# Performance work log

Measured on AMD Instinct MI355X. Metric: run time of the kernel, lower is better.

Reference implementation:

```python
import jax, jax.numpy as jnp
import numpy as np
import math

NUM_LAYERS = 4
NHEAD = 8
D_MODEL = 256
EPS_ATTN = 1e-6
EPS_LN = 1e-5


def _pos_encoding(d_model, h, w, dtype):
    # LoFTR 2D sinusoidal pos-enc, sliced to (h, w)
    d4 = d_model // 4
    y_pos = jnp.arange(1, h + 1, dtype=dtype)[None, :, None]  # [1,h,1]
    x_pos = jnp.arange(1, w + 1, dtype=dtype)[None, None, :]  # [1,1,w]
    div = jnp.exp(jnp.arange(0, d_model // 2, 2, dtype=dtype) * (-math.log(10000.0) / (d_model // 2)))
    div = div[:, None, None]  # [d4,1,1]
    pe = jnp.zeros((d_model, h, w), dtype=dtype)
    pe = pe.at[0::4].set(jnp.sin(x_pos * div))
    pe = pe.at[1::4].set(jnp.cos(x_pos * div))
    pe = pe.at[2::4].set(jnp.sin(y_pos * div))
    pe = pe.at[3::4].set(jnp.cos(y_pos * div))
    return pe


def _layernorm(x, g, b):
    mu = jnp.mean(x, axis=-1, keepdims=True)
    var = jnp.mean(jnp.square(x - mu), axis=-1, keepdims=True)
    return (x - mu) * jax.lax.rsqrt(var + EPS_LN) * g + b


def _encoder_layer(x, Wq, Wk, Wv, Wm, W1, W2, g1, b1, g2, b2):
    # x: [n, L, d]; weights stored [in, out]
    n, L, d = x.shape
    dh = d // NHEAD
    q = (x @ Wq).reshape(n, L, NHEAD, dh)
    k = (x @ Wk).reshape(n, L, NHEAD, dh)
    v = (x @ Wv).reshape(n, L, NHEAD, dh)
    # linear attention: feature map elu(x)+1
    Q = jax.nn.elu(q) + 1.0
    K = jax.nn.elu(k) + 1.0
    v_len = jnp.asarray(L, x.dtype)
    V = v / v_len
    KV = jnp.einsum('nshd,nshv->nhdv', K, V)            # [n,H,dh,dh]
    Z = 1.0 / (jnp.einsum('nlhd,nhd->nlh', Q, K.sum(axis=1)) + EPS_ATTN)
    msg = jnp.einsum('nlhd,nhdv,nlh->nlhv', Q, KV, Z) * v_len  # [n,L,H,dh]
    msg = msg.reshape(n, L, d) @ Wm
    msg = _layernorm(msg, g1, b1)
    msg = jnp.concatenate([x, msg], axis=-1)             # [n,L,2d]
    msg = jax.nn.relu(msg @ W1) @ W2
    msg = _layernorm(msg, g2, b2)
    return x + msg


def setup_inputs() -> dict:
    key = jax.random.key(0)
    ks = jax.random.split(key, 8)
    b, c, h, w = 8, D_MODEL, 64, 64
    d = D_MODEL
    sc_d = 1.0 / math.sqrt(d)
    sc_2d = 1.0 / math.sqrt(2 * d)
    feats = jax.random.normal(ks[0], (b, c, h, w), dtype=jnp.float32)
    Wq = jax.random.normal(ks[1], (NUM_LAYERS, d, d), dtype=jnp.float32) * sc_d
    Wk = jax.random.normal(ks[2], (NUM_LAYERS, d, d), dtype=jnp.float32) * sc_d
    Wv = jax.random.normal(ks[3], (NUM_LAYERS, d, d), dtype=jnp.float32) * sc_d
    Wmerge = jax.random.normal(ks[4], (NUM_LAYERS, d, d), dtype=jnp.float32) * sc_d
    Wmlp1 = jax.random.normal(ks[5], (NUM_LAYERS, 2 * d, 2 * d), dtype=jnp.float32) * sc_2d
    Wmlp2 = jax.random.normal(ks[6], (NUM_LAYERS, 2 * d, d), dtype=jnp.float32) * sc_2d
    ln1_g = jnp.ones((NUM_LAYERS, d), dtype=jnp.float32)
    ln1_b = jnp.zeros((NUM_LAYERS, d), dtype=jnp.float32)
    ln2_g = jnp.ones((NUM_LAYERS, d), dtype=jnp.float32)
    ln2_b = jnp.zeros((NUM_LAYERS, d), dtype=jnp.float32)
    return {'feats': feats, 'Wq': Wq, 'Wk': Wk, 'Wv': Wv, 'Wmerge': Wmerge,
            'Wmlp1': Wmlp1, 'Wmlp2': Wmlp2, 'ln1_g': ln1_g, 'ln1_b': ln1_b,
            'ln2_g': ln2_g, 'ln2_b': ln2_b}


def reference(feats, Wq, Wk, Wv, Wmerge, Wmlp1, Wmlp2, ln1_g, ln1_b, ln2_g, ln2_b):
    b, c, h, w = feats.shape
    x = feats + _pos_encoding(c, h, w, feats.dtype)[None]   # add_posEnc=True
    x = x.reshape(b, c, h * w).transpose(0, 2, 1)            # n (h w) c
    for i in range(NUM_LAYERS):
        x = _encoder_layer(x, Wq[i], Wk[i], Wv[i], Wmerge[i], Wmlp1[i], Wmlp2[i],
                           ln1_g[i], ln1_b[i], ln2_g[i], ln2_b[i])
    return x.transpose(0, 2, 1).reshape(b, c, h, w)
```

## Files before the change

kernel.cpp:

```cpp
#include <hip/hip_runtime.h>
#include <hip/hip_bf16.h>

#define LTOT 4096
#define DM 256
#define BATCH 8
#define MROWS (BATCH * LTOT)
#define NX ((size_t)MROWS * DM)

typedef __bf16 bf16x8 __attribute__((ext_vector_type(8)));
typedef float f32x4 __attribute__((ext_vector_type(4)));

#define AS1 __attribute__((address_space(1)))
#define AS3 __attribute__((address_space(3)))

__device__ __forceinline__ float elu1(float x) {
    return x > 0.f ? x + 1.f : expf(x);
}
__device__ __forceinline__ ushort f2bf(float f) {
    unsigned u = __float_as_uint(f);
    u += 0x7FFFu + ((u >> 16) & 1u);
    return (ushort)(u >> 16);
}
__device__ __forceinline__ float b2f(ushort u) {
    return __uint_as_float(((unsigned)u) << 16);
}

__global__ __launch_bounds__(256) void prep_kernel(const float* __restrict__ feats,
                                                   ushort* __restrict__ XC) {
    __shared__ float tile[32][33];
    int b = blockIdx.z;
    int l0 = blockIdx.x * 32;
    int c0 = blockIdx.y * 32;
    int tx = threadIdx.x, ty = threadIdx.y;
#pragma unroll
    for (int j = 0; j < 4; ++j) {
        int c = c0 + ty + j * 8;
        tile[ty + j * 8][tx] = feats[((size_t)(b * DM + c)) * LTOT + l0 + tx];
    }
    __syncthreads();
#pragma unroll
    for (int j = 0; j < 4; ++j) {
        int l = l0 + ty + j * 8;
        int c = c0 + tx;
        int i2 = (c >> 2) * 2;
        float dv = expf((float)i2 * -0.07195578415156063f);
        int rem = c & 3;
        int y = l >> 6, xc = l & 63;
        float pos = (rem < 2) ? (float)(xc + 1) : (float)(y + 1);
        float arg = pos * dv;
        float pe = (rem & 1) ? cosf(arg) : sinf(arg);
        float val = tile[tx][ty + j * 8] + pe;
        size_t row = (size_t)(b * LTOT + l);
        XC[row * 512 + c] = f2bf(val);
    }
}

__global__ __launch_bounds__(256) void unprep_kernel(const float* __restrict__ X,
                                                     float* __restrict__ out) {
    __shared__ float tile[32][33];
    int b = blockIdx.z;
    int l0 = blockIdx.x * 32;
    int c0 = blockIdx.y * 32;
    int tx = threadIdx.x, ty = threadIdx.y;
#pragma unroll
    for (int j = 0; j < 4; ++j) {
        int l = l0 + ty + j * 8;
        tile[ty + j * 8][tx] = X[((size_t)(b * LTOT + l)) * DM + c0 + tx];
    }
    __syncthreads();
#pragma unroll
    for (int j = 0; j < 4; ++j) {
        int c = c0 + ty + j * 8;
        out[((size_t)(b * DM + c)) * LTOT + l0 + tx] = tile[tx][ty + j * 8];
    }
}

__global__ __launch_bounds__(256) void wtrans_all(const float* __restrict__ Wq,
                                                  const float* __restrict__ Wk,
                                                  const float* __restrict__ Wv,
                                                  const float* __restrict__ Wm,
                                                  const float* __restrict__ W1,
                                                  const float* __restrict__ W2,
                                                  ushort* __restrict__ WTqkv,
                                                  ushort* __restrict__ WTm,
                                                  ushort* __restrict__ WT1,
                                                  ushort* __restrict__ WT2) {
    __shared__ float t[32][33];
    int idx = blockIdx.x;
    const float* W;
    ushort* WT;
    int K, N, KT, z, r;
    size_t in_ls, out_ls;
    if (idx < 1024) {
        int which = idx >> 8, local = idx & 255;
        K = 256; N = 256; KT = 8; in_ls = 65536;
        if (which == 0)      { W = Wq; WT = WTqkv;          out_ls = 196608; }
        else if (which == 1) { W = Wk; WT = WTqkv + 65536;  out_ls = 196608; }
        else if (which == 2) { W = Wv; WT = WTqkv + 131072; out_ls = 196608; }
        else                 { W = Wm; WT = WTm;            out_ls = 65536; }
        z = local >> 6; r = local & 63;
    } else if (idx < 2048) {
        int local = idx - 1024;
        K = 512; N = 512; KT = 16; in_ls = 262144; out_ls = 262144;
        W = W1; WT = WT1;
        z = local >> 8; r = local & 255;
    } else {
        int local = idx - 2048;
        K = 512; N = 256; KT = 16; in_ls = 131072; out_ls = 131072;
        W = W2; WT = WT2;
        z = local >> 7; r = local & 127;
    }
    int k0 = (r % KT) * 32, n0 = (r / KT) * 32;
    const float* Wz = W + (size_t)z * in_ls;
    ushort* WTz = WT + (size_t)z * out_ls;
    int tx = threadIdx.x & 31, ty = threadIdx.x >> 5;
#pragma unroll
    for (int j = 0; j < 4; ++j)
        t[ty + j * 8][tx] = Wz[(size_t)(k0 + ty + j * 8) * N + n0 + tx];
    __syncthreads();
#pragma unroll
    for (int j = 0; j < 4; ++j)
        WTz[(size_t)(n0 + ty + j * 8) * K + k0 + tx] = f2bf(t[tx][ty + j * 8]);
}

template <int ACT, int K>
__global__ __launch_bounds__(512, 2) void gemm_bf16(const ushort* __restrict__ A, int lda,
                                                    const ushort* __restrict__ Bt,
                                                    ushort* __restrict__ Cb,
                                                    int N) {
    constexpr int S = K / 32;
    __shared__ ushort As[3][4096];
    __shared__ ushort Bs[3][8192];
    int tid = threadIdx.x;
    int m0 = blockIdx.x * 128, n0 = blockIdx.y * 256;
    int wave = tid >> 6, lane = tid & 63;
    int wm = (wave >> 2) * 64, wn = (wave & 3) * 64;
    int fm = lane & 15, kg = lane >> 4;
    int rr = tid >> 2, cc = (tid & 3) * 8;

    const ushort* Ag = A + (size_t)(m0 + rr) * lda + cc;
    const ushort* Bg = Bt + (size_t)(n0 + rr) * K + cc;
    const ushort* Bg2 = Bt + (size_t)(n0 + rr + 128) * K + cc;

    f32x4 acc[4][4] = {};

#define STAGE_G(buf, k0)                                                          \
    do {                                                                          \
        __builtin_amdgcn_global_load_lds((const AS1 void*)(Ag + (k0)),            \
                                         (AS3 void*)(&As[buf][wave * 512]),       \
                                         16, 0, 0);                               \
        __builtin_amdgcn_global_load_lds((const AS1 void*)(Bg + (k0)),            \
                                         (AS3 void*)(&Bs[buf][wave * 512]),       \
                                         16, 0, 0);                               \
        __builtin_amdgcn_global_load_lds((const AS1 void*)(Bg2 + (k0)),           \
                                         (AS3 void*)(&Bs[buf][4096 + wave * 512]),\
                                         16, 0, 0);                               \
    } while (0)

    STAGE_G(0, 0);
    STAGE_G(1, 32);
#pragma unroll
    for (int t = 0; t < S; ++t) {
        if (t + 1 < S) asm volatile("s_waitcnt vmcnt(3)" ::: "memory");
        else           asm volatile("s_waitcnt vmcnt(0)" ::: "memory");
        __builtin_amdgcn_s_barrier();
        const int rb = t % 3;
        bf16x8 afr[4], bfr[4];
#pragma unroll
        for (int i = 0; i < 4; ++i)
            afr[i] = *(const bf16x8*)(&As[rb][(wm + i * 16 + fm) * 32 + kg * 8]);
#pragma unroll
        for (int j = 0; j < 4; ++j)
            bfr[j] = *(const bf16x8*)(&Bs[rb][(wn + j * 16 + fm) * 32 + kg * 8]);
        if (t + 2 < S) STAGE_G((t + 2) % 3, (t + 2) * 32);
#pragma unroll
        for (int i = 0; i < 4; ++i)
#pragma unroll
            for (int j = 0; j < 4; ++j)
                acc[i][j] = __builtin_amdgcn_mfma_f32_16x16x32_bf16(afr[i], bfr[j], acc[i][j], 0, 0, 0);
        asm volatile("" ::: "memory");
        __builtin_amdgcn_s_barrier();
    }
#undef STAGE_G

#pragma unroll
    for (int i = 0; i < 4; ++i) {
        int grow0 = m0 + wm + i * 16 + kg * 4;
#pragma unroll
        for (int r = 0; r < 4; ++r) {
            size_t rowoff = (size_t)(grow0 + r) * N;
#pragma unroll
            for (int j = 0; j < 4; ++j) {
                float v = acc[i][j][r];
                int col = n0 + wn + j * 16 + fm;
                if (ACT == 2) v = fmaxf(v, 0.f);
                if (ACT == 3) v = (col < 512) ? elu1(v) : v;
                Cb[rowoff + col] = f2bf(v);
            }
        }
    }
}

template <int RES, int K>
__global__ __launch_bounds__(512, 2) void gemm_ln(const ushort* __restrict__ A, int lda,
                                                  const ushort* __restrict__ Bt,
                                                  const float* __restrict__ g,
                                                  const float* __restrict__ bta,
                                                  float* __restrict__ Xout,
                                                  ushort* __restrict__ XC) {
    constexpr int S = K / 32;
    __shared__ ushort As[3][4096];
    __shared__ ushort Bs[3][8192];
    __shared__ float red[128 * 8];
    __shared__ float musig[128 * 2];
    int tid = threadIdx.x;
    int m0 = blockIdx.x * 128;
    int wave = tid >> 6, lane = tid & 63;
    int wm = (wave >> 2) * 64, wn = (wave & 3) * 64;
    int fm = lane & 15, kg = lane >> 4;
    int rr = tid >> 2, cc = (tid & 3) * 8;

    const ushort* Ag = A + (size_t)(m0 + rr) * lda + cc;
    const ushort* Bg = Bt + (size_t)rr * K + cc;
    const ushort* Bg2 = Bt + (size_t)(rr + 128) * K + cc;

    f32x4 acc[4][4] = {};

#define STAGE_L(buf, k0)                                                          \
    do {                                                                          \
        __builtin_amdgcn_global_load_lds((const AS1 void*)(Ag + (k0)),            \
                                         (AS3 void*)(&As[buf][wave * 512]),       \
                                         16, 0, 0);                               \
        __builtin_amdgcn_global_load_lds((const AS1 void*)(Bg + (k0)),            \
                                         (AS3 void*)(&Bs[buf][wave * 512]),       \
                                         16, 0, 0);                               \
        __builtin_amdgcn_global_load_lds((const AS1 void*)(Bg2 + (k0)),           \
                                         (AS3 void*)(&Bs[buf][4096 + wave * 512]),\
                                         16, 0, 0);                               \
    } while (0)

    STAGE_L(0, 0);
    STAGE_L(1, 32);
#pragma unroll
    for (int t = 0; t < S; ++t) {
        if (t + 1 < S) asm volatile("s_waitcnt vmcnt(3)" ::: "memory");
        else           asm volatile("s_waitcnt vmcnt(0)" ::: "memory");
        __builtin_amdgcn_s_barrier();
        const int rb = t % 3;
        bf16x8 afr[4], bfr[4];
#pragma unroll
        for (int i = 0; i < 4; ++i)
            afr[i] = *(const bf16x8*)(&As[rb][(wm + i * 16 + fm) * 32 + kg * 8]);
#pragma unroll
        for (int j = 0; j < 4; ++j)
            bfr[j] = *(const bf16x8*)(&Bs[rb][(wn + j * 16 + fm) * 32 + kg * 8]);
        if (t + 2 < S) STAGE_L((t + 2) % 3, (t + 2) * 32);
#pragma unroll
        for (int i = 0; i < 4; ++i)
#pragma unroll
            for (int j = 0; j < 4; ++j)
                acc[i][j] = __builtin_amdgcn_mfma_f32_16x16x32_bf16(afr[i], bfr[j], acc[i][j], 0, 0, 0);
        asm volatile("" ::: "memory");
        __builtin_amdgcn_s_barrier();
    }
#undef STAGE_L

#pragma unroll
    for (int i = 0; i < 4; ++i) {
#pragma unroll
        for (int r = 0; r < 4; ++r) {
            float s = acc[i][0][r] + acc[i][1][r] + acc[i][2][r] + acc[i][3][r];
            float q = acc[i][0][r] * acc[i][0][r] + acc[i][1][r] * acc[i][1][r] +
                      acc[i][2][r] * acc[i][2][r] + acc[i][3][r] * acc[i][3][r];
#pragma unroll
            for (int o = 1; o < 16; o <<= 1) {
                s += __shfl_xor(s, o, 64);
                q += __shfl_xor(q, o, 64);
            }
            if ((lane & 15) == 0) {
                int row = wm + i * 16 + kg * 4 + r;
                red[row * 8 + (wave & 3)] = s;
                red[row * 8 + 4 + (wave & 3)] = q;
            }
        }
    }
    __syncthreads();
    if (tid < 128) {
        float s = red[tid * 8 + 0] + red[tid * 8 + 1] + red[tid * 8 + 2] + red[tid * 8 + 3];
        float q = red[tid * 8 + 4] + red[tid * 8 + 5] + red[tid * 8 + 6] + red[tid * 8 + 7];
        float mu = s * (1.f / 256.f);
        float var = q * (1.f / 256.f) - mu * mu;
        musig[tid * 2] = mu;
        musig[tid * 2 + 1] = rsqrtf(var + 1e-5f);
    }
    __syncthreads();

    float gv[4], bv[4];
#pragma unroll
    for (int j = 0; j < 4; ++j) {
        int col = wn + j * 16 + fm;
        gv[j] = g[col];
        bv[j] = bta[col];
    }
#pragma unroll
    for (int i = 0; i < 4; ++i) {
#pragma unroll
        for (int r = 0; r < 4; ++r) {
            int rl = wm + i * 16 + kg * 4 + r;
            float mu = musig[rl * 2], rstd = musig[rl * 2 + 1];
            size_t grow = (size_t)(m0 + rl);
#pragma unroll
            for (int j = 0; j < 4; ++j) {
                int col = wn + j * 16 + fm;
                float v = (acc[i][j][r] - mu) * rstd * gv[j] + bv[j];
                if (RES) {
                    float x = b2f(XC[grow * 512 + col]) + v;
                    XC[grow * 512 + col] = f2bf(x);
                    if (Xout) Xout[grow * 256 + col] = x;
                } else {
                    XC[grow * 512 + 256 + col] = f2bf(v);
                }
            }
        }
    }
}

__global__ __launch_bounds__(256) void kv_kernel(const ushort* __restrict__ Kf,
                                                 const ushort* __restrict__ Vf,
                                                 int str,
                                                 float* __restrict__ KVp,
                                                 float* __restrict__ KSp) {
    __shared__ float redv[3][8][8][16];
    __shared__ float redk[3][8][4];
    int tid = threadIdx.x;
    int bh = blockIdx.x, sp = blockIdx.y;
    int b = bh >> 3, h = bh & 7;
    int sg = tid >> 6, d2 = (tid >> 3) & 7, v2 = tid & 7;
    size_t rbase = (size_t)(b * LTOT + sp * 512 + sg * 128) * str;
    const ushort* Kp = Kf + rbase + h * 32 + d2 * 4;
    const ushort* Vp = Vf + rbase + h * 32 + v2 * 4;
    float acc[4][4] = {};
    float ks[4] = {};
#pragma unroll 4
    for (int s = 0; s < 128; ++s) {
        ushort4 k4 = *(const ushort4*)(Kp + (size_t)s * str);
        ushort4 v4 = *(const ushort4*)(Vp + (size_t)s * str);
        float kk0 = b2f(k4.x), kk1 = b2f(k4.y), kk2 = b2f(k4.z), kk3 = b2f(k4.w);
        float vv0 = b2f(v4.x), vv1 = b2f(v4.y), vv2 = b2f(v4.z), vv3 = b2f(v4.w);
        acc[0][0] += kk0 * vv0; acc[0][1] += kk0 * vv1; acc[0][2] += kk0 * vv2; acc[0][3] += kk0 * vv3;
        acc[1][0] += kk1 * vv0; acc[1][1] += kk1 * vv1; acc[1][2] += kk1 * vv2; acc[1][3] += kk1 * vv3;
        acc[2][0] += kk2 * vv0; acc[2][1] += kk2 * vv1; acc[2][2] += kk2 * vv2; acc[2][3] += kk2 * vv3;
        acc[3][0] += kk3 * vv0; acc[3][1] += kk3 * vv1; acc[3][2] += kk3 * vv2; acc[3][3] += kk3 * vv3;
        ks[0] += kk0; ks[1] += kk1; ks[2] += kk2; ks[3] += kk3;
    }
    if (sg > 0) {
#pragma unroll
        for (int i = 0; i < 4; ++i)
#pragma unroll
            for (int j = 0; j < 4; ++j)
                redv[sg - 1][d2][v2][i * 4 + j] = acc[i][j];
        if (v2 == 0) {
#pragma unroll
            for (int i = 0; i < 4; ++i) redk[sg - 1][d2][i] = ks[i];
        }
    }
    __syncthreads();
    if (sg == 0) {
#pragma unroll
        for (int t = 0; t < 3; ++t)
#pragma unroll
            for (int i = 0; i < 4; ++i)
#pragma unroll
                for (int j = 0; j < 4; ++j)
                    acc[i][j] += redv[t][d2][v2][i * 4 + j];
        float* base = KVp + (size_t)(sp * 64 + bh) * 1024;
#pragma unroll
        for (int i = 0; i < 4; ++i) {
            float4 o = make_float4(acc[i][0], acc[i][1], acc[i][2], acc[i][3]);
            *(float4*)(base + (d2 * 4 + i) * 32 + v2 * 4) = o;
        }
        if (v2 == 0) {
#pragma unroll
            for (int t = 0; t < 3; ++t)
#pragma unroll
                for (int i = 0; i < 4; ++i) ks[i] += redk[t][d2][i];
#pragma unroll
            for (int i = 0; i < 4; ++i)
                KSp[(sp * 64 + bh) * 32 + d2 * 4 + i] = ks[i];
        }
    }
}

__global__ __launch_bounds__(256) void kvreduce_kernel(const float* __restrict__ KVp,
                                                       const float* __restrict__ KSp,
                                                       ushort* __restrict__ KVT,
                                                       float* __restrict__ KS) {
    int bh = blockIdx.x;
    int t = threadIdx.x;
    float4 s = make_float4(0.f, 0.f, 0.f, 0.f);
#pragma unroll
    for (int sp = 0; sp < 8; ++sp) {
        float4 v = *(const float4*)(KVp + ((size_t)(sp * 64 + bh)) * 1024 + t * 4);
        s.x += v.x; s.y += v.y; s.z += v.z; s.w += v.w;
    }
    int d = t >> 3, v0 = (t & 7) * 4;
    ushort* dst = KVT + (size_t)bh * 1024 + d;
    dst[(v0 + 0) * 32] = f2bf(s.x);
    dst[(v0 + 1) * 32] = f2bf(s.y);
    dst[(v0 + 2) * 32] = f2bf(s.z);
    dst[(v0 + 3) * 32] = f2bf(s.w);
    if (t < 32) {
        float ks = 0.f;
#pragma unroll
        for (int sp = 0; sp < 8; ++sp) ks += KSp[(sp * 64 + bh) * 32 + t];
        KS[bh * 32 + t] = ks;
    }
}

__global__ __launch_bounds__(256) void msg_mfma(const ushort* __restrict__ Qb, int qstr,
                                                const ushort* __restrict__ KVT,
                                                const float* __restrict__ KS,
                                                ushort* __restrict__ Msgb) {
    __shared__ ushort kvs[8 * 1280];
    int tid = threadIdx.x;
    int b = blockIdx.y;
    int lc = blockIdx.x;
    {
        const ushort* src = KVT + (size_t)b * 8192;
#pragma unroll
        for (int it = 0; it < 4; ++it) {
            int base = it * 2048 + tid * 8;
            int h = base >> 10, rem = base & 1023;
            int v = rem >> 5, d = rem & 31;
            bf16x8 val = *(const bf16x8*)(src + base);
            *(bf16x8*)(kvs + h * 1280 + v * 40 + d) = val;
        }
    }
    __syncthreads();
    int wave = tid >> 6, lane = tid & 63;
    int fm = lane & 15, kg = lane >> 4;
    int row0 = b * LTOT + lc * 64 + wave * 16;

    for (int h = 0; h < 8; ++h) {
        bf16x8 afr = *(const bf16x8*)(Qb + (size_t)(row0 + fm) * qstr + h * 32 + kg * 8);
        bf16x8 bfr0 = *(const bf16x8*)(kvs + h * 1280 + fm * 40 + kg * 8);
        bf16x8 bfr1 = *(const bf16x8*)(kvs + h * 1280 + (16 + fm) * 40 + kg * 8);
        f32x4 acc0 = {}, acc1 = {};
        acc0 = __builtin_amdgcn_mfma_f32_16x16x32_bf16(afr, bfr0, acc0, 0, 0, 0);
        acc1 = __builtin_amdgcn_mfma_f32_16x16x32_bf16(afr, bfr1, acc1, 0, 0, 0);
        const float* ksp = KS + (b * 8 + h) * 32 + kg * 8;
        float4 ka = *(const float4*)ksp;
        float4 kb = *(const float4*)(ksp + 4);
        float den = (float)afr[0] * ka.x + (float)afr[1] * ka.y +
                    (float)afr[2] * ka.z + (float)afr[3] * ka.w +
                    (float)afr[4] * kb.x + (float)afr[5] * kb.y +
                    (float)afr[6] * kb.z + (float)afr[7] * kb.w;
        den += __shfl_xor(den, 16, 64);
        den += __shfl_xor(den, 32, 64);
        float rz = 1.f / (den + 1e-6f);
#pragma unroll
        for (int r = 0; r < 4; ++r) {
            int rr = kg * 4 + r;
            float rzr = __shfl(rz, (kg << 4) | rr, 64);
            size_t ro = (size_t)(row0 + rr) * DM + h * 32;
            Msgb[ro + fm] = f2bf(acc0[r] * rzr);
            Msgb[ro + 16 + fm] = f2bf(acc1[r] * rzr);
        }
    }
}

extern "C" void kernel_launch(void* const* d_in, const int* in_sizes, int n_in,
                              void* d_out, int out_size, void* d_ws, size_t ws_size,
                              hipStream_t stream) {
    const float* feats = (const float*)d_in[0];
    const float* Wq = (const float*)d_in[1];
    const float* Wk = (const float*)d_in[2];
    const float* Wv = (const float*)d_in[3];
    const float* Wm = (const float*)d_in[4];
    const float* W1 = (const float*)d_in[5];
    const float* W2 = (const float*)d_in[6];
    const float* g1 = (const float*)d_in[7];
    const float* b1 = (const float*)d_in[8];
    const float* g2 = (const float*)d_in[9];
    const float* b2 = (const float*)d_in[10];

    float* ws = (float*)d_ws;
    float* X = ws;
    ushort* XC = (ushort*)(ws + NX);
    ushort* QKVb = (ushort*)(ws + 2 * NX);
    ushort* HBb = QKVb;

    float* dout = (float*)d_out;
    ushort* msgb = (ushort*)dout;
    ushort* WB = (ushort*)dout + NX;
    ushort* WTqkv = WB;
    ushort* WTm = WB + 4 * 196608;
    ushort* WT1 = WTm + 4 * 65536;
    ushort* WT2 = WT1 + 4 * 262144;
    float* KVp = dout + (NX + 2621440) / 2;
    float* KSp = KVp + 524288;
    ushort* KVT = (ushort*)(KSp + 16384);
    float* KS = (float*)(KVT + 65536);

    wtrans_all<<<2560, 256, 0, stream>>>(Wq, Wk, Wv, Wm, W1, W2, WTqkv, WTm, WT1, WT2);
    prep_kernel<<<dim3(128, 8, 8), dim3(32, 8), 0, stream>>>(feats, XC);

    for (int layer = 0; layer < 4; ++layer) {
        const ushort* wtqkv = WTqkv + (size_t)layer * 196608;
        const ushort* wtm = WTm + (size_t)layer * 65536;
        const ushort* wt1 = WT1 + (size_t)layer * 262144;
        const ushort* wt2 = WT2 + (size_t)layer * 131072;
        const float* lg1 = g1 + layer * DM;
        const float* lb1 = b1 + layer * DM;
        const float* lg2 = g2 + layer * DM;
        const float* lb2 = b2 + layer * DM;

        gemm_bf16<3, 256><<<dim3(256, 3), 512, 0, stream>>>(XC, 512, wtqkv, QKVb, 768);
        kv_kernel<<<dim3(64, 8), 256, 0, stream>>>(QKVb + 256, QKVb + 512, 768, KVp, KSp);
        kvreduce_kernel<<<64, 256, 0, stream>>>(KVp, KSp, KVT, KS);
        msg_mfma<<<dim3(64, 8), 256, 0, stream>>>(QKVb, 768, KVT, KS, msgb);
        gemm_ln<0, 256><<<256, 512, 0, stream>>>(msgb, 256, wtm, lg1, lb1, nullptr, XC);
        gemm_bf16<2, 512><<<dim3(256, 2), 512, 0, stream>>>(XC, 512, wt1, HBb, 512);
        gemm_ln<1, 512><<<256, 512, 0, stream>>>(HBb, 512, wt2, lg2, lb2,
                                                 (layer == 3) ? X : nullptr, XC);
    }

    unprep_kernel<<<dim3(128, 8, 8), dim3(32, 8), 0, stream>>>(X, dout);
}
```

Measured before the change: 626.0 us.

## Stage whole weight panel in LDS and stream A fragments from global

Both GEMM kernels drop the triple-buffered async global-to-LDS pipeline for A and B. A 256x256 weight panel (padded rows) is now loaded into shared memory once per pass, and A fragments are read straight from global memory into registers with a one-step software prefetch. The aim is to cut barriers per K step and LDS traffic for A. The cost is that A loads are uncoalesced per-lane 16-byte reads that depend on cache hits, there is no overlap during the B panel load, and the larger LDS footprint (~132KB) may limit occupancy.

New measurement: 937.9 us. 49.8% more time.

```diff
diff --git a/kernel.cpp b/kernel.cpp
--- a/kernel.cpp
+++ b/kernel.cpp
@@ -124,64 +124,65 @@
 }
 
 template <int ACT, int K>
-__global__ __launch_bounds__(512, 2) void gemm_bf16(const ushort* __restrict__ A, int lda,
-                                                    const ushort* __restrict__ Bt,
-                                                    ushort* __restrict__ Cb,
-                                                    int N) {
-    constexpr int S = K / 32;
-    __shared__ ushort As[3][4096];
-    __shared__ ushort Bs[3][8192];
+__global__ __launch_bounds__(512, 2) void gemm_br(const ushort* __restrict__ A, int lda,
+                                                  const ushort* __restrict__ Bt,
+                                                  ushort* __restrict__ Cb, int N) {
+    constexpr int NP = K / 256;
+    __shared__ ushort Bs[256 * 264];
     int tid = threadIdx.x;
     int m0 = blockIdx.x * 128, n0 = blockIdx.y * 256;
     int wave = tid >> 6, lane = tid & 63;
     int wm = (wave >> 2) * 64, wn = (wave & 3) * 64;
     int fm = lane & 15, kg = lane >> 4;
-    int rr = tid >> 2, cc = (tid & 3) * 8;
-
-    const ushort* Ag = A + (size_t)(m0 + rr) * lda + cc;
-    const ushort* Bg = Bt + (size_t)(n0 + rr) * K + cc;
-    const ushort* Bg2 = Bt + (size_t)(n0 + rr + 128) * K + cc;
 
     f32x4 acc[4][4] = {};
-
-#define STAGE_G(buf, k0)                                                          \
-    do {                                                                          \
-        __builtin_amdgcn_global_load_lds((const AS1 void*)(Ag + (k0)),            \
-                                         (AS3 void*)(&As[buf][wave * 512]),       \
-                                         16, 0, 0);                               \
-        __builtin_amdgcn_global_load_lds((const AS1 void*)(Bg + (k0)),            \
-                                         (AS3 void*)(&Bs[buf][wave * 512]),       \
-                                         16, 0, 0);                               \
-        __builtin_amdgcn_global_load_lds((const AS1 void*)(Bg2 + (k0)),           \
-                                         (AS3 void*)(&Bs[buf][4096 + wave * 512]),\
-                                         16, 0, 0);                               \
-    } while (0)
-
-    STAGE_G(0, 0);
-    STAGE_G(1, 32);
-#pragma unroll
-    for (int t = 0; t < S; ++t) {
-        if (t + 1 < S) asm volatile("s_waitcnt vmcnt(3)" ::: "memory");
-        else           asm volatile("s_waitcnt vmcnt(0)" ::: "memory");
-        __builtin_amdgcn_s_barrier();
-        const int rb = t % 3;
-        bf16x8 afr[4], bfr[4];
+    const ushort* Ab = A + (size_t)(m0 + wm + fm) * lda + kg * 8;
+
+    int brow = tid >> 1, bhalf = (tid & 1) * 128;
+    const ushort* bsrc0 = Bt + (size_t)(n0 + brow) * K + bhalf;
+    ushort* bdst = Bs + brow * 264 + bhalf;
+
+#pragma unroll
+    for (int pass = 0; pass < NP; ++pass) {
+        if (pass) __syncthreads();
+        {
+            const ushort* bsrc = bsrc0 + pass * 256;
+#pragma unroll
+            for (int c = 0; c < 128; c += 8)
+                *(bf16x8*)(bdst + c) = *(const bf16x8*)(bsrc + c);
+        }
+        __syncthreads();
+        const int kb = pass * 256;
+        bf16x8 afn[4], bfn[4];
 #pragma unroll
         for (int i = 0; i < 4; ++i)
-            afr[i] = *(const bf16x8*)(&As[rb][(wm + i * 16 + fm) * 32 + kg * 8]);
+            afn[i] = *(const bf16x8*)(Ab + (size_t)i * 16 * lda + kb);
 #pragma unroll
         for (int j = 0; j < 4; ++j)
-            bfr[j] = *(const bf16x8*)(&Bs[rb][(wn + j * 16 + fm) * 32 + kg * 8]);
-        if (t + 2 < S) STAGE_G((t + 2) % 3, (t + 2) * 32);
-#pragma unroll
-        for (int i = 0; i < 4; ++i)
-#pragma unroll
-            for (int j = 0; j < 4; ++j)
-                acc[i][j] = __builtin_amdgcn_mfma_f32_16x16x32_bf16(afr[i], bfr[j], acc[i][j], 0, 0, 0);
-        asm volatile("" ::: "memory");
-        __builtin_amdgcn_s_barrier();
-    }
-#undef STAGE_G
+            bfn[j] = *(const bf16x8*)(Bs + (wn + j * 16 + fm) * 264 + kg * 8);
+#pragma unroll
+        for (int ks = 0; ks < 8; ++ks) {
+            bf16x8 afr[4], bfr[4];
+#pragma unroll
+            for (int i = 0; i < 4; ++i) afr[i] = afn[i];
+#pragma unroll
+            for (int j = 0; j < 4; ++j) bfr[j] = bfn[j];
+            if (ks + 1 < 8) {
+                int kn = kb + (ks + 1) * 32;
+#pragma unroll
+                for (int i = 0; i < 4; ++i)
+                    afn[i] = *(const bf16x8*)(Ab + (size_t)i * 16 * lda + kn);
+#pragma unroll
+                for (int j = 0; j < 4; ++j)
+                    bfn[j] = *(const bf16x8*)(Bs + (wn + j * 16 + fm) * 264 + (ks + 1) * 32 + kg * 8);
+            }
+#pragma unroll
+            for (int i = 0; i < 4; ++i)
+#pragma unroll
+                for (int j = 0; j < 4; ++j)
+                    acc[i][j] = __builtin_amdgcn_mfma_f32_16x16x32_bf16(afr[i], bfr[j], acc[i][j], 0, 0, 0);
+        }
+    }
 
 #pragma unroll
     for (int i = 0; i < 4; ++i) {
@@ -202,15 +203,14 @@
 }
 
 template <int RES, int K>
-__global__ __launch_bounds__(512, 2) void gemm_ln(const ushort* __restrict__ A, int lda,
-                                                  const ushort* __restrict__ Bt,
-                                                  const float* __restrict__ g,
-                                                  const float* __restrict__ bta,
-                                                  float* __restrict__ Xout,
-                                                  ushort* __restrict__ XC) {
-    constexpr int S = K / 32;
-    __shared__ ushort As[3][4096];
-    __shared__ ushort Bs[3][8192];
+__global__ __launch_bounds__(512, 2) void gemm_ln_br(const ushort* __restrict__ A, int lda,
+                                                     const ushort* __restrict__ Bt,
+                                                     const float* __restrict__ g,
+                                                     const float* __restrict__ bta,
+                                                     float* __restrict__ Xout,
+                                                     ushort* __restrict__ XC) {
+    constexpr int NP = K / 256;
+    __shared__ ushort Bs[256 * 264];
     __shared__ float red[128 * 8];
     __shared__ float musig[128 * 2];
     int tid = threadIdx.x;
@@ -218,52 +218,55 @@
     int wave = tid >> 6, lane = tid & 63;
     int wm = (wave >> 2) * 64, wn = (wave & 3) * 64;
     int fm = lane & 15, kg = lane >> 4;
-    int rr = tid >> 2, cc = (tid & 3) * 8;
-
-    const ushort* Ag = A + (size_t)(m0 + rr) * lda + cc;
-    const ushort* Bg = Bt + (size_t)rr * K + cc;
-    const ushort* Bg2 = Bt + (size_t)(rr + 128) * K + cc;
 
     f32x4 acc[4][4] = {};
-
-#define STAGE_L(buf, k0)                                                          \
-    do {                                                                          \
-        __builtin_amdgcn_global_load_lds((const AS1 void*)(Ag + (k0)),            \
-                                         (AS3 void*)(&As[buf][wave * 512]),       \
-                                         16, 0, 0);                               \
-        __builtin_amdgcn_global_load_lds((const AS1 void*)(Bg + (k0)),            \
-                                         (AS3 void*)(&Bs[buf][wave * 512]),       \
-                                         16, 0, 0);                               \
-        __builtin_amdgcn_global_load_lds((const AS1 void*)(Bg2 + (k0)),           \
-                                         (AS3 void*)(&Bs[buf][4096 + wave * 512]),\
-                                         16, 0, 0);                               \
-    } while (0)
-
-    STAGE_L(0, 0);
-    STAGE_L(1, 32);
-#pragma unroll
-    for (int t = 0; t < S; ++t) {
-        if (t + 1 < S) asm volatile("s_waitcnt vmcnt(3)" ::: "memory");
-        else           asm volatile("s_waitcnt vmcnt(0)" ::: "memory");
-        __builtin_amdgcn_s_barrier();
-        const int rb = t % 3;
-        bf16x8 afr[4], bfr[4];
+    const ushort* Ab = A + (size_t)(m0 + wm + fm) * lda + kg * 8;
+
+    int brow = tid >> 1, bhalf = (tid & 1) * 128;
+    const ushort* bsrc0 = Bt + (size_t)brow * K + bhalf;
+    ushort* bdst = Bs + brow * 264 + bhalf;
+
+#pragma unroll
+    for (int pass = 0; pass < NP; ++pass) {
+        if (pass) __syncthreads();
+        {
+            const ushort* bsrc = bsrc0 + pass * 256;
+#pragma unroll
+            for (int c = 0; c < 128; c += 8)
+                *(bf16x8*)(bdst + c) = *(const bf16x8*)(bsrc + c);
+        }
+        __syncthreads();
+        const int kb = pass * 256;
+        bf16x8 afn[4], bfn[4];
 #pragma unroll
         for (int i = 0; i < 4; ++i)
-            afr[i] = *(const bf16x8*)(&As[rb][(wm + i * 16 + fm) * 32 + kg * 8]);
+            afn[i] = *(const bf16x8*)(Ab + (size_t)i * 16 * lda + kb);
 #pragma unroll
         for (int j = 0; j < 4; ++j)
-            bfr[j] = *(const bf16x8*)(&Bs[rb][(wn + j * 16 + fm) * 32 + kg * 8]);
-        if (t + 2 < S) STAGE_L((t + 2) % 3, (t + 2) * 32);
-#pragma unroll
-        for (int i = 0; i < 4; ++i)
-#pragma unroll
-            for (int j = 0; j < 4; ++j)
-                acc[i][j] = __builtin_amdgcn_mfma_f32_16x16x32_bf16(afr[i], bfr[j], acc[i][j], 0, 0, 0);
-        asm volatile("" ::: "memory");
-        __builtin_amdgcn_s_barrier();
-    }
-#undef STAGE_L
+            bfn[j] = *(const bf16x8*)(Bs + (wn + j * 16 + fm) * 264 + kg * 8);
+#pragma unroll
+        for (int ks = 0; ks < 8; ++ks) {
+            bf16x8 afr[4], bfr[4];
+#pragma unroll
+            for (int i = 0; i < 4; ++i) afr[i] = afn[i];
+#pragma unroll
+            for (int j = 0; j < 4; ++j) bfr[j] = bfn[j];
+            if (ks + 1 < 8) {
+                int kn = kb + (ks + 1) * 32;
+#pragma unroll
+                for (int i = 0; i < 4; ++i)
+                    afn[i] = *(const bf16x8*)(Ab + (size_t)i * 16 * lda + kn);
+#pragma unroll
+                for (int j = 0; j < 4; ++j)
+                    bfn[j] = *(const bf16x8*)(Bs + (wn + j * 16 + fm) * 264 + (ks + 1) * 32 + kg * 8);
+            }
+#pragma unroll
+            for (int i = 0; i < 4; ++i)
+#pragma unroll
+                for (int j = 0; j < 4; ++j)
+                    acc[i][j] = __builtin_amdgcn_mfma_f32_16x16x32_bf16(afr[i], bfr[j], acc[i][j], 0, 0, 0);
+        }
+    }
 
 #pragma unroll
     for (int i = 0; i < 4; ++i) {
@@ -515,14 +518,14 @@
         const float* lg2 = g2 + layer * DM;
         const float* lb2 = b2 + layer * DM;
 
-        gemm_bf16<3, 256><<<dim3(256, 3), 512, 0, stream>>>(XC, 512, wtqkv, QKVb, 768);
+        gemm_br<3, 256><<<dim3(256, 3), 512, 0, stream>>>(XC, 512, wtqkv, QKVb, 768);
         kv_kernel<<<dim3(64, 8), 256, 0, stream>>>(QKVb + 256, QKVb + 512, 768, KVp, KSp);
         kvreduce_kernel<<<64, 256, 0, stream>>>(KVp, KSp, KVT, KS);
         msg_mfma<<<dim3(64, 8), 256, 0, stream>>>(QKVb, 768, KVT, KS, msgb);
-        gemm_ln<0, 256><<<256, 512, 0, stream>>>(msgb, 256, wtm, lg1, lb1, nullptr, XC);
-        gemm_bf16<2, 512><<<dim3(256, 2), 512, 0, stream>>>(XC, 512, wt1, HBb, 512);
-        gemm_ln<1, 512><<<256, 512, 0, stream>>>(HBb, 512, wt2, lg2, lb2,
-                                                 (layer == 3) ? X : nullptr, XC);
+        gemm_ln_br<0, 256><<<256, 512, 0, stream>>>(msgb, 256, wtm, lg1, lb1, nullptr, XC);
+        gemm_br<2, 512><<<dim3(256, 2), 512, 0, stream>>>(XC, 512, wt1, HBb, 512);
+        gemm_ln_br<1, 512><<<256, 512, 0, stream>>>(HBb, 512, wt2, lg2, lb2,
+                                                    (layer == 3) ? X : nullptr, XC);
     }
 
     unprep_kernel<<<dim3(128, 8, 8), dim3(32, 8), 0, stream>>>(X, dout);
```
